# Performance work log

Hardware: AMD Instinct MI355X
Metric: run time of the kernel (lower is better)

The kernel has to match this reference:

```python
import jax, jax.numpy as jnp
import numpy as np

EPS = 1e-12

def _l2_normalize(v, axis):
    norm = jnp.linalg.norm(v, ord=2, axis=axis, keepdims=True)
    return v / jnp.maximum(norm, EPS)

def setup_inputs() -> dict:
    key = jax.random.key(0)
    k1, k2, k3 = jax.random.split(key, 3)
    B, H, W, D, K = 16, 56, 56, 512, 32
    x = jax.random.normal(k1, (B, H, W, D), dtype=jnp.float32)
    # 1x1 conv weight (no bias): equivalent to a (D,K) matmul; he_normal-ish scale
    Wc = jax.random.normal(k2, (D, K), dtype=jnp.float32) * jnp.sqrt(2.0 / D)
    # cluster centers, original shape (1,1,1,512,32) -> stored as (D,K)
    C = jax.random.normal(k3, (D, K), dtype=jnp.float32) * jnp.sqrt(2.0 / D)
    return {"x": x, "Wc": Wc, "C": C}

def reference(x, Wc, C):
    # soft-assignment: 1x1 conv + softmax over clusters
    s = jnp.einsum('bhwd,dk->bhwk', x, Wc)          # (B,H,W,K)
    a = jax.nn.softmax(s, axis=-1)                   # (B,H,W,K)
    # v[b,d,k] = sum_{h,w} a[b,h,w,k] * (x[b,h,w,d] + C[d,k])
    #          = einsum(a,x) + C * sum_{h,w} a   (avoids (B,H,W,D,K) intermediate)
    ax = jnp.einsum('bhwk,bhwd->bdk', a, x)          # (B,D,K)
    a_sum = jnp.sum(a, axis=(1, 2))                  # (B,K)
    v = ax + C[None, :, :] * a_sum[:, None, :]       # (B,D,K)
    # intra-normalize over cluster axis (dim=2), flatten, L2 normalize
    v = _l2_normalize(v, axis=2)
    v = v.reshape(v.shape[0], -1)                    # (B, D*K)
    return _l2_normalize(v, axis=1)
```

## Files before the change

kernel.cpp:

```cpp
#include <hip/hip_runtime.h>
#include <math.h>


#define BATCH 16
#define HW    3136
#define DIM   512
#define KCL   32
#define NCHK  49
#define SLABF (BATCH * DIM * KCL + 256)

typedef __attribute__((ext_vector_type(8))) short short8;
typedef __attribute__((ext_vector_type(4))) float f32x4;

__device__ __forceinline__ void atomAddF(float* p, float v) {
    unsafeAtomicAdd(p, v);
}

__device__ __forceinline__ unsigned short f2bf(float f) {
    unsigned u = __float_as_uint(f);
    return (unsigned short)((u + 0x7FFFu + ((u >> 16) & 1u)) >> 16);
}

#define XS_STR  136
#define WTC_STR 136
#define AT_STR  72
#define XT_STR  72

__global__ __launch_bounds__(256, 5) void k_sax(const float* __restrict__ x,
                                                const float* __restrict__ Wc,
                                                float* __restrict__ vpart,
                                                float* __restrict__ a_sum) {
    __shared__ unsigned short xs[9216];
    __shared__ unsigned short wt[32 * WTC_STR];
    __shared__ unsigned short aT[KCL * AT_STR];
    __shared__ float asum_l[4][32];
    const int t    = threadIdx.x;
    const int lane = t & 63;
    const int wv   = t >> 6;
    const int l15  = lane & 15;
    const int quad = lane >> 4;
    const int n0   = blockIdx.x * 64;
    const int b    = n0 / HW;
    const int ch   = blockIdx.x % NCHK;

    float4 px[8];
#pragma unroll
    for (int i = 0; i < 8; ++i) {
        int f = i * 256 + t;
        px[i] = *(const float4*)(x + ((size_t)(n0 + (f >> 5)) * DIM + (f & 31) * 4));
    }

    f32x4 acc0 = {0.f, 0.f, 0.f, 0.f};
    f32x4 acc1 = {0.f, 0.f, 0.f, 0.f};

    for (int c = 0; c < 4; ++c) {
        const int dc = c * 128;
        float4 wc4[4];
#pragma unroll
        for (int i = 0; i < 4; ++i) {
            int f = i * 256 + t;
            wc4[i] = *(const float4*)(Wc + (size_t)(dc + (f >> 3)) * KCL + (f & 7) * 4);
        }
        __syncthreads();
#pragma unroll
        for (int i = 0; i < 8; ++i) {
            int f = i * 256 + t;
            ushort4 w;
            w.x = f2bf(px[i].x); w.y = f2bf(px[i].y);
            w.z = f2bf(px[i].z); w.w = f2bf(px[i].w);
            *(ushort4*)&xs[(f >> 5) * XS_STR + (f & 31) * 4] = w;
        }
#pragma unroll
        for (int i = 0; i < 4; ++i) {
            int f  = i * 256 + t;
            int d  = f >> 3;
            int k4 = (f & 7) * 4;
            wt[(k4 + 0) * WTC_STR + d] = f2bf(wc4[i].x);
            wt[(k4 + 1) * WTC_STR + d] = f2bf(wc4[i].y);
            wt[(k4 + 2) * WTC_STR + d] = f2bf(wc4[i].z);
            wt[(k4 + 3) * WTC_STR + d] = f2bf(wc4[i].w);
        }
        __syncthreads();
        if (c < 3) {
            const int dn = dc + 128;
#pragma unroll
            for (int i = 0; i < 8; ++i) {
                int f = i * 256 + t;
                px[i] = *(const float4*)(x + ((size_t)(n0 + (f >> 5)) * DIM + dn + (f & 31) * 4));
            }
        }
#pragma unroll
        for (int ds = 0; ds < 4; ++ds) {
            const int dloc = ds * 32 + quad * 8;
            short8 af = *(const short8*)&xs[(wv * 16 + l15) * XS_STR + dloc];
            short8 b0 = *(const short8*)&wt[l15 * WTC_STR + dloc];
            short8 b1 = *(const short8*)&wt[(16 + l15) * WTC_STR + dloc];
            acc0 = __builtin_amdgcn_mfma_f32_16x16x32_bf16(af, b0, acc0, 0, 0, 0);
            acc1 = __builtin_amdgcn_mfma_f32_16x16x32_bf16(af, b1, acc1, 0, 0, 0);
        }
    }

    float at0 = 0.f, at1 = 0.f;
#pragma unroll
    for (int r = 0; r < 4; ++r) {
        float m = fmaxf(acc0[r], acc1[r]);
        m = fmaxf(m, __shfl_xor(m, 1));
        m = fmaxf(m, __shfl_xor(m, 2));
        m = fmaxf(m, __shfl_xor(m, 4));
        m = fmaxf(m, __shfl_xor(m, 8));
        float e0 = __expf(acc0[r] - m);
        float e1 = __expf(acc1[r] - m);
        float s = e0 + e1;
        s += __shfl_xor(s, 1);
        s += __shfl_xor(s, 2);
        s += __shfl_xor(s, 4);
        s += __shfl_xor(s, 8);
        float inv = 1.f / s;
        float a0 = e0 * inv, a1 = e1 * inv;
        const int pos = wv * 16 + quad * 4 + r;
        aT[l15 * AT_STR + pos]        = f2bf(a0);
        aT[(16 + l15) * AT_STR + pos] = f2bf(a1);
        at0 += a0; at1 += a1;
    }
    at0 += __shfl_xor(at0, 16); at0 += __shfl_xor(at0, 32);
    at1 += __shfl_xor(at1, 16); at1 += __shfl_xor(at1, 32);
    if (quad == 0) {
        asum_l[wv][l15]      = at0;
        asum_l[wv][16 + l15] = at1;
    }

    const int dl  = t & 127;
    const int pg0 = t >> 7;
    const float* xb = x + (size_t)n0 * DIM + dl;
    float pf[32];
#pragma unroll
    for (int i = 0; i < 8; ++i) {
        const int p = (pg0 + 2 * i) * 4;
#pragma unroll
        for (int j = 0; j < 4; ++j)
            pf[i * 4 + j] = xb[(size_t)(p + j) * DIM];
    }

    __syncthreads();
    if (t < 32)
        atomAddF(&a_sum[b * KCL + t],
                 asum_l[0][t] + asum_l[1][t] + asum_l[2][t] + asum_l[3][t]);

    float* vp = vpart + (size_t)ch * SLABF + (size_t)b * DIM * KCL;
    for (int dc = 0; dc < DIM; dc += 128) {
        __syncthreads();
#pragma unroll
        for (int i = 0; i < 8; ++i) {
            const int p = (pg0 + 2 * i) * 4;
            ushort4 w;
            w.x = f2bf(pf[i * 4 + 0]);
            w.y = f2bf(pf[i * 4 + 1]);
            w.z = f2bf(pf[i * 4 + 2]);
            w.w = f2bf(pf[i * 4 + 3]);
            *(ushort4*)&xs[dl * XT_STR + (p ^ (((dl >> 3) & 7) << 3))] = w;
        }
        __syncthreads();
        if (dc < 384) {
            const int dn = dc + 128;
#pragma unroll
            for (int i = 0; i < 8; ++i) {
                const int p = (pg0 + 2 * i) * 4;
#pragma unroll
                for (int j = 0; j < 4; ++j)
                    pf[i * 4 + j] = xb[(size_t)(p + j) * DIM + dn];
            }
        }
        f32x4 z = {0.f, 0.f, 0.f, 0.f};
        f32x4 pacc[2][2];
        pacc[0][0] = z; pacc[0][1] = z; pacc[1][0] = z; pacc[1][1] = z;
#pragma unroll
        for (int s = 0; s < 2; ++s) {
            const int pb = s * 32 + quad * 8;
            short8 bf0 = *(const short8*)&aT[l15 * AT_STR + pb];
            short8 bf1 = *(const short8*)&aT[(16 + l15) * AT_STR + pb];
#pragma unroll
            for (int m2 = 0; m2 < 2; ++m2) {
                const int dloc = (wv * 2 + m2) * 16 + l15;
                short8 af = *(const short8*)&xs[dloc * XT_STR + (pb ^ (((dloc >> 3) & 7) << 3))];
                pacc[m2][0] = __builtin_amdgcn_mfma_f32_16x16x32_bf16(af, bf0, pacc[m2][0], 0, 0, 0);
                pacc[m2][1] = __builtin_amdgcn_mfma_f32_16x16x32_bf16(af, bf1, pacc[m2][1], 0, 0, 0);
            }
        }
#pragma unroll
        for (int m2 = 0; m2 < 2; ++m2) {
            const int dr = dc + (wv * 2 + m2) * 16 + quad * 4;
#pragma unroll
            for (int r = 0; r < 4; ++r) {
                vp[(size_t)(dr + r) * KCL + l15]      = pacc[m2][0][r];
                vp[(size_t)(dr + r) * KCL + 16 + l15] = pacc[m2][1][r];
            }
        }
    }
}

__global__ __launch_bounds__(128) void k_norm1(const float* __restrict__ vpart,
                                               const float* __restrict__ a_sum,
                                               const float* __restrict__ Cc,
                                               float* __restrict__ out,
                                               float* __restrict__ ssq, int PS) {
    const int t = threadIdx.x;
    const int row = blockIdx.x * 4 + (t >> 5);
    const int k = t & 31;
    const int b = row >> 9;
    const int d = row & 511;

    float sum = 0.f;
    for (int ps = 0; ps < PS; ++ps)
        sum += vpart[(size_t)ps * SLABF + (size_t)row * KCL + k];
    float v = sum + Cc[d * KCL + k] * a_sum[b * KCL + k];

    float ss = v * v;
    ss += __shfl_xor(ss, 1, 32);  ss += __shfl_xor(ss, 2, 32);
    ss += __shfl_xor(ss, 4, 32);  ss += __shfl_xor(ss, 8, 32);
    ss += __shfl_xor(ss, 16, 32);
    float inv = 1.f / fmaxf(sqrtf(ss), 1e-12f);
    float r = v * inv;
    out[(size_t)row * KCL + k] = r;

    float bs = r * r;
    for (int off = 32; off > 0; off >>= 1) bs += __shfl_down(bs, off, 64);
    __shared__ float red[2];
    if ((t & 63) == 0) red[t >> 6] = bs;
    __syncthreads();
    if (t == 0) atomAddF(&ssq[b], red[0] + red[1]);
}

__global__ __launch_bounds__(256) void k_norm2(float* __restrict__ out,
                                               const float* __restrict__ ssq) {
    const int i4 = blockIdx.x * 256 + threadIdx.x;
    const int b = i4 >> 12;
    float inv = 1.f / fmaxf(sqrtf(ssq[b]), 1e-12f);
    float4 v = *(float4*)(out + (size_t)i4 * 4);
    v.x *= inv; v.y *= inv; v.z *= inv; v.w *= inv;
    *(float4*)(out + (size_t)i4 * 4) = v;
}

extern "C" void kernel_launch(void* const* d_in, const int* in_sizes, int n_in,
                              void* d_out, int out_size, void* d_ws, size_t ws_size,
                              hipStream_t stream) {
    const float* x  = (const float*)d_in[0];
    const float* Wc = (const float*)d_in[1];
    const float* Cc = (const float*)d_in[2];
    float* out = (float*)d_out;

    char* ws = (char*)d_ws;
    float* vpart = (float*)ws;
    float* a_sum = (float*)(ws + (size_t)NCHK * SLABF * 4);
    float* ssq   = (float*)(ws + (size_t)NCHK * SLABF * 4 + 2048);

    hipMemsetAsync(a_sum, 0, 2048 + 64, stream);

    k_sax  <<<784, 256, 0, stream>>>(x, Wc, vpart, a_sum);
    k_norm1<<<2048, 128, 0, stream>>>(vpart, a_sum, Cc, out, ssq, NCHK);
    k_norm2<<<256, 256, 0, stream>>>(out, ssq);
}
```

Baseline: 216.4 us.

## Double-buffer global loads in k_sax and unroll partial-sum reduction in k_norm1

Both GEMM phases of k_sax now use two register buffers, so loads for chunk c+2 are in flight while chunk c is staged and computed. This gives a deeper prefetch than the old single-buffer scheme. The occupancy hint drops from 5 to 3 blocks per CU to make room for the extra registers. k_norm1 now uses 256-thread blocks and unrolls the 49-slab reduction with four independent accumulators to expose more memory-level parallelism. The cost is higher register pressure and lower occupancy in k_sax.

```diff
diff --git a/kernel.cpp b/kernel.cpp
--- a/kernel.cpp
+++ b/kernel.cpp
@@ -26,7 +26,104 @@
 #define AT_STR  72
 #define XT_STR  72
 
-__global__ __launch_bounds__(256, 5) void k_sax(const float* __restrict__ x,
+#define LOAD_PX(PX, DC)                                                        \
+    _Pragma("unroll")                                                          \
+    for (int i = 0; i < 8; ++i) {                                              \
+        int f = i * 256 + t;                                                   \
+        PX[i] = *(const float4*)(x + ((size_t)(n0 + (f >> 5)) * DIM + (DC) + (f & 31) * 4)); \
+    }
+
+#define LOAD_WC(WC, DC)                                                        \
+    _Pragma("unroll")                                                          \
+    for (int i = 0; i < 4; ++i) {                                              \
+        int f = i * 256 + t;                                                   \
+        WC[i] = *(const float4*)(Wc + (size_t)((DC) + (f >> 3)) * KCL + (f & 7) * 4); \
+    }
+
+#define P1_STAGE(PX, WC)                                                       \
+    __syncthreads();                                                           \
+    _Pragma("unroll")                                                          \
+    for (int i = 0; i < 8; ++i) {                                              \
+        int f = i * 256 + t;                                                   \
+        ushort4 w;                                                             \
+        w.x = f2bf(PX[i].x); w.y = f2bf(PX[i].y);                              \
+        w.z = f2bf(PX[i].z); w.w = f2bf(PX[i].w);                              \
+        *(ushort4*)&xs[(f >> 5) * XS_STR + (f & 31) * 4] = w;                  \
+    }                                                                          \
+    _Pragma("unroll")                                                          \
+    for (int i = 0; i < 4; ++i) {                                              \
+        int f  = i * 256 + t;                                                  \
+        int d  = f >> 3;                                                       \
+        int k4 = (f & 7) * 4;                                                  \
+        wt[(k4 + 0) * WTC_STR + d] = f2bf(WC[i].x);                            \
+        wt[(k4 + 1) * WTC_STR + d] = f2bf(WC[i].y);                            \
+        wt[(k4 + 2) * WTC_STR + d] = f2bf(WC[i].z);                            \
+        wt[(k4 + 3) * WTC_STR + d] = f2bf(WC[i].w);                            \
+    }                                                                          \
+    __syncthreads();
+
+#define P1_MFMA()                                                              \
+    _Pragma("unroll")                                                          \
+    for (int ds_ = 0; ds_ < 4; ++ds_) {                                        \
+        const int dloc = ds_ * 32 + quad * 8;                                  \
+        short8 af = *(const short8*)&xs[(wv * 16 + l15) * XS_STR + dloc];      \
+        short8 b0 = *(const short8*)&wt[l15 * WTC_STR + dloc];                 \
+        short8 b1 = *(const short8*)&wt[(16 + l15) * WTC_STR + dloc];          \
+        acc0 = __builtin_amdgcn_mfma_f32_16x16x32_bf16(af, b0, acc0, 0, 0, 0); \
+        acc1 = __builtin_amdgcn_mfma_f32_16x16x32_bf16(af, b1, acc1, 0, 0, 0); \
+    }
+
+#define LOAD_PF(PF, DC)                                                        \
+    _Pragma("unroll")                                                          \
+    for (int i = 0; i < 8; ++i) {                                              \
+        const int p = (pg0 + 2 * i) * 4;                                       \
+        _Pragma("unroll")                                                      \
+        for (int j = 0; j < 4; ++j)                                            \
+            PF[i * 4 + j] = xb[(size_t)(p + j) * DIM + (DC)];                  \
+    }
+
+#define P2_STAGE(PF)                                                           \
+    __syncthreads();                                                           \
+    _Pragma("unroll")                                                          \
+    for (int i = 0; i < 8; ++i) {                                              \
+        const int p = (pg0 + 2 * i) * 4;                                       \
+        ushort4 w;                                                             \
+        w.x = f2bf(PF[i * 4 + 0]); w.y = f2bf(PF[i * 4 + 1]);                  \
+        w.z = f2bf(PF[i * 4 + 2]); w.w = f2bf(PF[i * 4 + 3]);                  \
+        *(ushort4*)&xs[dl * XT_STR + (p ^ (((dl >> 3) & 7) << 3))] = w;        \
+    }                                                                          \
+    __syncthreads();
+
+#define P2_MFMA_STORE(DC)                                                      \
+    {                                                                          \
+        f32x4 z = {0.f, 0.f, 0.f, 0.f};                                        \
+        f32x4 pacc[2][2];                                                      \
+        pacc[0][0] = z; pacc[0][1] = z; pacc[1][0] = z; pacc[1][1] = z;        \
+        _Pragma("unroll")                                                      \
+        for (int s_ = 0; s_ < 2; ++s_) {                                       \
+            const int pb = s_ * 32 + quad * 8;                                 \
+            short8 bf0 = *(const short8*)&aT[l15 * AT_STR + pb];               \
+            short8 bf1 = *(const short8*)&aT[(16 + l15) * AT_STR + pb];        \
+            _Pragma("unroll")                                                  \
+            for (int m2 = 0; m2 < 2; ++m2) {                                   \
+                const int dloc = (wv * 2 + m2) * 16 + l15;                     \
+                short8 af = *(const short8*)&xs[dloc * XT_STR + (pb ^ (((dloc >> 3) & 7) << 3))]; \
+                pacc[m2][0] = __builtin_amdgcn_mfma_f32_16x16x32_bf16(af, bf0, pacc[m2][0], 0, 0, 0); \
+                pacc[m2][1] = __builtin_amdgcn_mfma_f32_16x16x32_bf16(af, bf1, pacc[m2][1], 0, 0, 0); \
+            }                                                                  \
+        }                                                                      \
+        _Pragma("unroll")                                                      \
+        for (int m2 = 0; m2 < 2; ++m2) {                                       \
+            const int dr = (DC) + (wv * 2 + m2) * 16 + quad * 4;               \
+            _Pragma("unroll")                                                  \
+            for (int r = 0; r < 4; ++r) {                                      \
+                vp[(size_t)(dr + r) * KCL + l15]      = pacc[m2][0][r];        \
+                vp[(size_t)(dr + r) * KCL + 16 + l15] = pacc[m2][1][r];        \
+            }                                                                  \
+        }                                                                      \
+    }
+
+__global__ __launch_bounds__(256, 3) void k_sax(const float* __restrict__ x,
                                                 const float* __restrict__ Wc,
                                                 float* __restrict__ vpart,
                                                 float* __restrict__ a_sum) {
@@ -43,62 +140,23 @@
     const int b    = n0 / HW;
     const int ch   = blockIdx.x % NCHK;
 
-    float4 px[8];
-#pragma unroll
-    for (int i = 0; i < 8; ++i) {
-        int f = i * 256 + t;
-        px[i] = *(const float4*)(x + ((size_t)(n0 + (f >> 5)) * DIM + (f & 31) * 4));
-    }
-
     f32x4 acc0 = {0.f, 0.f, 0.f, 0.f};
     f32x4 acc1 = {0.f, 0.f, 0.f, 0.f};
 
-    for (int c = 0; c < 4; ++c) {
-        const int dc = c * 128;
-        float4 wc4[4];
-#pragma unroll
-        for (int i = 0; i < 4; ++i) {
-            int f = i * 256 + t;
-            wc4[i] = *(const float4*)(Wc + (size_t)(dc + (f >> 3)) * KCL + (f & 7) * 4);
-        }
-        __syncthreads();
-#pragma unroll
-        for (int i = 0; i < 8; ++i) {
-            int f = i * 256 + t;
-            ushort4 w;
-            w.x = f2bf(px[i].x); w.y = f2bf(px[i].y);
-            w.z = f2bf(px[i].z); w.w = f2bf(px[i].w);
-            *(ushort4*)&xs[(f >> 5) * XS_STR + (f & 31) * 4] = w;
-        }
-#pragma unroll
-        for (int i = 0; i < 4; ++i) {
-            int f  = i * 256 + t;
-            int d  = f >> 3;
-            int k4 = (f & 7) * 4;
-            wt[(k4 + 0) * WTC_STR + d] = f2bf(wc4[i].x);
-            wt[(k4 + 1) * WTC_STR + d] = f2bf(wc4[i].y);
-            wt[(k4 + 2) * WTC_STR + d] = f2bf(wc4[i].z);
-            wt[(k4 + 3) * WTC_STR + d] = f2bf(wc4[i].w);
-        }
-        __syncthreads();
-        if (c < 3) {
-            const int dn = dc + 128;
-#pragma unroll
-            for (int i = 0; i < 8; ++i) {
-                int f = i * 256 + t;
-                px[i] = *(const float4*)(x + ((size_t)(n0 + (f >> 5)) * DIM + dn + (f & 31) * 4));
-            }
-        }
-#pragma unroll
-        for (int ds = 0; ds < 4; ++ds) {
-            const int dloc = ds * 32 + quad * 8;
-            short8 af = *(const short8*)&xs[(wv * 16 + l15) * XS_STR + dloc];
-            short8 b0 = *(const short8*)&wt[l15 * WTC_STR + dloc];
-            short8 b1 = *(const short8*)&wt[(16 + l15) * WTC_STR + dloc];
-            acc0 = __builtin_amdgcn_mfma_f32_16x16x32_bf16(af, b0, acc0, 0, 0, 0);
-            acc1 = __builtin_amdgcn_mfma_f32_16x16x32_bf16(af, b1, acc1, 0, 0, 0);
-        }
-    }
+    float4 pxA[8], pxB[8], wcA[4], wcB[4];
+    LOAD_PX(pxA, 0);    LOAD_WC(wcA, 0);
+    LOAD_PX(pxB, 128);  LOAD_WC(wcB, 128);
+
+    P1_STAGE(pxA, wcA);
+    LOAD_PX(pxA, 256);  LOAD_WC(wcA, 256);
+    P1_MFMA();
+    P1_STAGE(pxB, wcB);
+    LOAD_PX(pxB, 384);  LOAD_WC(wcB, 384);
+    P1_MFMA();
+    P1_STAGE(pxA, wcA);
+    P1_MFMA();
+    P1_STAGE(pxB, wcB);
+    P1_MFMA();
 
     float at0 = 0.f, at1 = 0.f;
 #pragma unroll
@@ -132,87 +190,51 @@
     const int dl  = t & 127;
     const int pg0 = t >> 7;
     const float* xb = x + (size_t)n0 * DIM + dl;
-    float pf[32];
-#pragma unroll
-    for (int i = 0; i < 8; ++i) {
-        const int p = (pg0 + 2 * i) * 4;
-#pragma unroll
-        for (int j = 0; j < 4; ++j)
-            pf[i * 4 + j] = xb[(size_t)(p + j) * DIM];
-    }
+    float* vp = vpart + (size_t)ch * SLABF + (size_t)b * DIM * KCL;
+
+    float pfA[32], pfB[32];
+    LOAD_PF(pfA, 0);
+    LOAD_PF(pfB, 128);
 
     __syncthreads();
     if (t < 32)
         atomAddF(&a_sum[b * KCL + t],
                  asum_l[0][t] + asum_l[1][t] + asum_l[2][t] + asum_l[3][t]);
 
-    float* vp = vpart + (size_t)ch * SLABF + (size_t)b * DIM * KCL;
-    for (int dc = 0; dc < DIM; dc += 128) {
-        __syncthreads();
-#pragma unroll
-        for (int i = 0; i < 8; ++i) {
-            const int p = (pg0 + 2 * i) * 4;
-            ushort4 w;
-            w.x = f2bf(pf[i * 4 + 0]);
-            w.y = f2bf(pf[i * 4 + 1]);
-            w.z = f2bf(pf[i * 4 + 2]);
-            w.w = f2bf(pf[i * 4 + 3]);
-            *(ushort4*)&xs[dl * XT_STR + (p ^ (((dl >> 3) & 7) << 3))] = w;
-        }
-        __syncthreads();
-        if (dc < 384) {
-            const int dn = dc + 128;
-#pragma unroll
-            for (int i = 0; i < 8; ++i) {
-                const int p = (pg0 + 2 * i) * 4;
-#pragma unroll
-                for (int j = 0; j < 4; ++j)
-                    pf[i * 4 + j] = xb[(size_t)(p + j) * DIM + dn];
-            }
-        }
-        f32x4 z = {0.f, 0.f, 0.f, 0.f};
-        f32x4 pacc[2][2];
-        pacc[0][0] = z; pacc[0][1] = z; pacc[1][0] = z; pacc[1][1] = z;
-#pragma unroll
-        for (int s = 0; s < 2; ++s) {
-            const int pb = s * 32 + quad * 8;
-            short8 bf0 = *(const short8*)&aT[l15 * AT_STR + pb];
-            short8 bf1 = *(const short8*)&aT[(16 + l15) * AT_STR + pb];
-#pragma unroll
-            for (int m2 = 0; m2 < 2; ++m2) {
-                const int dloc = (wv * 2 + m2) * 16 + l15;
-                short8 af = *(const short8*)&xs[dloc * XT_STR + (pb ^ (((dloc >> 3) & 7) << 3))];
-                pacc[m2][0] = __builtin_amdgcn_mfma_f32_16x16x32_bf16(af, bf0, pacc[m2][0], 0, 0, 0);
-                pacc[m2][1] = __builtin_amdgcn_mfma_f32_16x16x32_bf16(af, bf1, pacc[m2][1], 0, 0, 0);
-            }
-        }
-#pragma unroll
-        for (int m2 = 0; m2 < 2; ++m2) {
-            const int dr = dc + (wv * 2 + m2) * 16 + quad * 4;
-#pragma unroll
-            for (int r = 0; r < 4; ++r) {
-                vp[(size_t)(dr + r) * KCL + l15]      = pacc[m2][0][r];
-                vp[(size_t)(dr + r) * KCL + 16 + l15] = pacc[m2][1][r];
-            }
-        }
-    }
-}
-
-__global__ __launch_bounds__(128) void k_norm1(const float* __restrict__ vpart,
+    P2_STAGE(pfA);
+    LOAD_PF(pfA, 256);
+    P2_MFMA_STORE(0);
+    P2_STAGE(pfB);
+    LOAD_PF(pfB, 384);
+    P2_MFMA_STORE(128);
+    P2_STAGE(pfA);
+    P2_MFMA_STORE(256);
+    P2_STAGE(pfB);
+    P2_MFMA_STORE(384);
+}
+
+__global__ __launch_bounds__(256) void k_norm1(const float* __restrict__ vpart,
                                                const float* __restrict__ a_sum,
                                                const float* __restrict__ Cc,
                                                float* __restrict__ out,
-                                               float* __restrict__ ssq, int PS) {
+                                               float* __restrict__ ssq) {
     const int t = threadIdx.x;
-    const int row = blockIdx.x * 4 + (t >> 5);
+    const int row = blockIdx.x * 8 + (t >> 5);
     const int k = t & 31;
     const int b = row >> 9;
     const int d = row & 511;
 
-    float sum = 0.f;
-    for (int ps = 0; ps < PS; ++ps)
-        sum += vpart[(size_t)ps * SLABF + (size_t)row * KCL + k];
-    float v = sum + Cc[d * KCL + k] * a_sum[b * KCL + k];
+    const float* vp = vpart + (size_t)row * KCL + k;
+    float s0 = 0.f, s1 = 0.f, s2 = 0.f, s3 = 0.f;
+#pragma unroll
+    for (int ps = 0; ps < 48; ps += 4) {
+        s0 += vp[(size_t)(ps + 0) * SLABF];
+        s1 += vp[(size_t)(ps + 1) * SLABF];
+        s2 += vp[(size_t)(ps + 2) * SLABF];
+        s3 += vp[(size_t)(ps + 3) * SLABF];
+    }
+    s0 += vp[(size_t)48 * SLABF];
+    float v = (s0 + s1) + (s2 + s3) + Cc[d * KCL + k] * a_sum[b * KCL + k];
 
     float ss = v * v;
     ss += __shfl_xor(ss, 1, 32);  ss += __shfl_xor(ss, 2, 32);
@@ -224,10 +246,10 @@
 
     float bs = r * r;
     for (int off = 32; off > 0; off >>= 1) bs += __shfl_down(bs, off, 64);
-    __shared__ float red[2];
+    __shared__ float red[4];
     if ((t & 63) == 0) red[t >> 6] = bs;
     __syncthreads();
-    if (t == 0) atomAddF(&ssq[b], red[0] + red[1]);
+    if (t == 0) atomAddF(&ssq[b], (red[0] + red[1]) + (red[2] + red[3]));
 }
 
 __global__ __launch_bounds__(256) void k_norm2(float* __restrict__ out,
@@ -256,6 +278,6 @@
     hipMemsetAsync(a_sum, 0, 2048 + 64, stream);
 
     k_sax  <<<784, 256, 0, stream>>>(x, Wc, vpart, a_sum);
-    k_norm1<<<2048, 128, 0, stream>>>(vpart, a_sum, Cc, out, ssq, NCHK);
+    k_norm1<<<1024, 256, 0, stream>>>(vpart, a_sum, Cc, out, ssq);
     k_norm2<<<256, 256, 0, stream>>>(out, ssq);
 }
```

Result: faster. 195.1 us (-9.8%).
